# Optimization experiments

Hardware: AMD Instinct MI355X
Metric: run time of the kernel (lower is better)

The kernel has to match this reference:

```python
import jax, jax.numpy as jnp
import numpy as np

B, T, C, H, S = 4, 1024, 768, 12, 64  # batch, seq, emb_dim, n_heads, head_size
FF = 4 * C          # 3072, ff_hidden_size (required by SwiGLU input dim)
HID = int(8 * C / 3)  # 2048, SwiGLU hidden
EPS = 1e-6


def _rope_tables(seq_len, dim):
    # theta = 10000 ** (-2 * arange(0, dim, 2) / dim)  (note extra factor 2 vs standard RoPE)
    theta = 10000.0 ** (-2.0 * jnp.arange(0, dim, 2, dtype=jnp.float32) / dim)
    freqs = jnp.arange(seq_len, dtype=jnp.float32)[:, None] * theta  # [T, dim/2]
    cos = jnp.repeat(jnp.cos(freqs), 2, axis=-1)  # [T, dim]
    sin = jnp.repeat(jnp.sin(freqs), 2, axis=-1)
    return cos, sin


def _rope(x, cos, sin):
    # x: [..., T, S]; rotate pairs: even' = -odd, odd' = even
    rot = jnp.stack([-x[..., 1::2], x[..., 0::2]], axis=-1).reshape(x.shape)
    return x * cos + rot * sin


def _rmsnorm(x, gamma):
    # global scalar RMS over the whole tensor (faithful to torch.mean with no dim)
    return x / jnp.sqrt(EPS + jnp.mean(x * x)) * gamma


def _block(x, Wq, Wk, Wv, Wo, g1, g2, W1, b1, Ww, bw, Wg, bg, Wd, bd, W2, b2):
    Tlen = x.shape[1]
    cos, sin = _rope_tables(Tlen, S)
    # --- multi-head attention on rms1(x) ---
    h = _rmsnorm(x, g1)
    q = jnp.einsum('btc,hcs->bhts', h, Wq)
    k = jnp.einsum('btc,hcs->bhts', h, Wk)
    v = jnp.einsum('btc,hcs->bhts', h, Wv)
    rq = _rope(q, cos, sin)
    rk = _rope(k, cos, sin)
    scores = jnp.einsum('bhts,bhks->bhtk', rq, rk) * (C ** -0.5)  # scale by emb_dim, faithful
    causal = jnp.tril(jnp.ones((Tlen, Tlen), dtype=bool))
    scores = jnp.where(causal, scores, -jnp.inf)
    probs = jax.nn.softmax(scores, axis=-1)
    attn = jnp.einsum('bhtk,bhks->bhts', probs, v)
    attn = attn.transpose(0, 2, 1, 3).reshape(x.shape[0], Tlen, C)  # concat heads
    out = x + attn @ Wo
    # --- feed forward on rms2(out) ---
    h2 = _rmsnorm(out, g2)
    u = h2 @ W1 + b1                      # [B,T,FF]
    wx = u @ Ww + bw                      # [B,T,HID]
    vx = u @ Wg + bg
    ff = (wx * (vx * jax.nn.sigmoid(vx))) @ Wd + bd  # [B,T,FF]
    ff = ff @ W2 + b2                     # [B,T,C]
    return out + ff


def setup_inputs() -> dict:
    key = jax.random.key(0)
    ks = jax.random.split(key, 17)
    sd = 0.02
    return {
        'x':  jax.random.normal(ks[0], (B, T, C), jnp.float32),
        'Wq': jax.random.normal(ks[1], (H, C, S), jnp.float32) * sd,
        'Wk': jax.random.normal(ks[2], (H, C, S), jnp.float32) * sd,
        'Wv': jax.random.normal(ks[3], (H, C, S), jnp.float32) * sd,
        'Wo': jax.random.normal(ks[4], (C, C), jnp.float32) * sd,
        'g1': jnp.ones((C,), jnp.float32),
        'g2': jnp.ones((C,), jnp.float32),
        'W1': jax.random.normal(ks[5], (C, FF), jnp.float32) * sd,
        'b1': jnp.zeros((FF,), jnp.float32),
        'Ww': jax.random.normal(ks[6], (FF, HID), jnp.float32) * sd,
        'bw': jnp.zeros((HID,), jnp.float32),
        'Wg': jax.random.normal(ks[7], (FF, HID), jnp.float32) * sd,
        'bg': jnp.zeros((HID,), jnp.float32),
        'Wd': jax.random.normal(ks[8], (HID, FF), jnp.float32) * sd,
        'bd': jnp.zeros((FF,), jnp.float32),
        'W2': jax.random.normal(ks[9], (FF, C), jnp.float32) * sd,
        'b2': jnp.zeros((C,), jnp.float32),
    }


def reference(x, Wq, Wk, Wv, Wo, g1, g2, W1, b1, Ww, bw, Wg, bg, Wd, bd, W2, b2):
    return _block(x, Wq, Wk, Wv, Wo, g1, g2, W1, b1, Ww, bw, Wg, bg, Wd, bd, W2, b2)
```

## Files before the change

### kernel.cpp

```cpp
#include <hip/hip_runtime.h>
#include <math.h>

#define BB   4
#define TT   1024
#define CC   768
#define HH   12
#define SS   64
#define FFD  3072
#define HIDD 2048
#define NTOK (BB*TT)
#define EPSR 1e-6f

typedef __attribute__((ext_vector_type(8))) short bf16x8;
typedef __attribute__((ext_vector_type(4))) float f32x4;

__device__ __forceinline__ unsigned short f2bf(float f) {
    unsigned u = __float_as_uint(f);
    return (unsigned short)((u + 0x7FFFu + ((u >> 16) & 1u)) >> 16);
}
__device__ __forceinline__ float bfl(unsigned u) { return __uint_as_float(u << 16); }
__device__ __forceinline__ float bfh(unsigned u) { return __uint_as_float(u & 0xFFFF0000u); }
__device__ __forceinline__ unsigned pk2(float a, float b) {
    return (unsigned)f2bf(a) | ((unsigned)f2bf(b) << 16);
}

__device__ __forceinline__ void gload_lds16(const unsigned short* g, unsigned short* l) {
    __builtin_amdgcn_global_load_lds(
        (const __attribute__((address_space(1))) unsigned int*)g,
        (__attribute__((address_space(3))) unsigned int*)l, 16, 0, 0);
}

__global__ void k_scale_gamma_b(const float* __restrict__ x, const float* __restrict__ g,
                                const float* __restrict__ part, unsigned short* __restrict__ h,
                                int n8, float invn, int npart) {
    __shared__ float sm[256];
    float s = 0.f;
    for (int i = threadIdx.x; i < npart; i += 256) s += part[i];
    sm[threadIdx.x] = s;
    __syncthreads();
    for (int off = 128; off > 0; off >>= 1) {
        if (threadIdx.x < off) sm[threadIdx.x] += sm[threadIdx.x + off];
        __syncthreads();
    }
    float sc = 1.0f / sqrtf(EPSR + sm[0] * invn);
    int i = blockIdx.x * blockDim.x + threadIdx.x;
    if (i >= n8) return;
    float4 v0 = ((const float4*)x)[2*i];
    float4 v1 = ((const float4*)x)[2*i+1];
    int c = (i * 8) % CC;
    float4 g0 = *(const float4*)(g + c);
    float4 g1v = *(const float4*)(g + c + 4);
    uint4 r;
    r.x = pk2(v0.x*sc*g0.x,  v0.y*sc*g0.y);
    r.y = pk2(v0.z*sc*g0.z,  v0.w*sc*g0.w);
    r.z = pk2(v1.x*sc*g1v.x, v1.y*sc*g1v.y);
    r.w = pk2(v1.z*sc*g1v.z, v1.w*sc*g1v.w);
    ((uint4*)h)[i] = r;
}

#define TQKV 1728
#define TWO  576
#define TW1  2304
#define TWW  6144
#define TWD  6144
#define TW2  2304
#define J0 (TQKV)
#define J1 (J0 + TWO)
#define J2 (J1 + TW1)
#define J3 (J2 + TWW)
#define J4 (J3 + TWW)
#define J5 (J4 + TWD)
#define J6 (J5 + TW2)
#define J7 (J6 + 16)
#define J8 (J7 + 128)
#define JSUM 1024
#define J9 (J8 + JSUM)

__device__ __forceinline__ void wT_tile(float (*tl)[33], const float* __restrict__ W,
                                        unsigned short* __restrict__ Wt,
                                        int K, int N, int t, int tx, int ty) {
    int nk = K >> 5;
    int k0 = (t % nk) * 32, n0 = (t / nk) * 32;
#pragma unroll
    for (int i = 0; i < 4; ++i)
        tl[ty + i*8][tx] = W[(size_t)(k0 + ty + i*8) * N + n0 + tx];
    __syncthreads();
#pragma unroll
    for (int i = 0; i < 4; ++i)
        Wt[(size_t)(n0 + ty + i*8) * K + k0 + tx] = f2bf(tl[tx][ty + i*8]);
}

__device__ __forceinline__ void wT_tile_il(float (*tl)[33], const float* __restrict__ W,
                                           unsigned short* __restrict__ Wt,
                                           int K, int N, int t, int tx, int ty, int ofs) {
    int nk = K >> 5;
    int k0 = (t % nk) * 32, n0 = (t / nk) * 32;
#pragma unroll
    for (int i = 0; i < 4; ++i)
        tl[ty + i*8][tx] = W[(size_t)(k0 + ty + i*8) * N + n0 + tx];
    __syncthreads();
#pragma unroll
    for (int i = 0; i < 4; ++i) {
        int j = n0 + ty + i*8;
        int pr = ((j & ~15) << 1) + ofs*16 + (j & 15);
        Wt[(size_t)pr * K + k0 + tx] = f2bf(tl[tx][ty + i*8]);
    }
}

__global__ void k_prep(const float* __restrict__ Wq, const float* __restrict__ Wk,
                       const float* __restrict__ Wv, const float* __restrict__ Wo,
                       const float* __restrict__ W1, const float* __restrict__ Ww,
                       const float* __restrict__ Wg, const float* __restrict__ Wd,
                       const float* __restrict__ W2, const float* __restrict__ bw,
                       const float* __restrict__ bg, const float* __restrict__ x,
                       unsigned short* __restrict__ wqkvT, unsigned short* __restrict__ WoT,
                       unsigned short* __restrict__ W1T, unsigned short* __restrict__ WcatT,
                       unsigned short* __restrict__ WdT, unsigned short* __restrict__ W2T,
                       float* __restrict__ bcat, float* __restrict__ tab,
                       float* __restrict__ part) {
    __shared__ float tl[32][33];
    const int bid = blockIdx.x;
    const int tx = threadIdx.x & 31, ty = threadIdx.x >> 5;
    if (bid < J0) {
        int t = bid;
        int c0 = (t % 24) * 32;
        int s0 = ((t / 24) & 1) * 32;
        int z = t / 48, sel = z / HH, h = z % HH;
        const float* W = (sel == 0 ? Wq : (sel == 1 ? Wk : Wv)) + (size_t)h * CC * SS;
#pragma unroll
        for (int i = 0; i < 4; ++i)
            tl[ty + i*8][tx] = W[(size_t)(c0 + ty + i*8) * SS + s0 + tx];
        __syncthreads();
#pragma unroll
        for (int i = 0; i < 4; ++i)
            wqkvT[(size_t)(sel*CC + h*SS + s0 + ty + i*8) * CC + c0 + tx] = f2bf(tl[tx][ty + i*8]);
    } else if (bid < J1) {
        wT_tile(tl, Wo, WoT, CC, CC, bid - J0, tx, ty);
    } else if (bid < J2) {
        wT_tile(tl, W1, W1T, CC, FFD, bid - J1, tx, ty);
    } else if (bid < J3) {
        wT_tile_il(tl, Ww, WcatT, FFD, HIDD, bid - J2, tx, ty, 0);
    } else if (bid < J4) {
        wT_tile_il(tl, Wg, WcatT, FFD, HIDD, bid - J3, tx, ty, 1);
    } else if (bid < J5) {
        wT_tile(tl, Wd, WdT, HIDD, FFD, bid - J4, tx, ty);
    } else if (bid < J6) {
        wT_tile(tl, W2, W2T, FFD, CC, bid - J5, tx, ty);
    } else if (bid < J7) {
        int ip = (bid - J6) * 256 + threadIdx.x;
        int lg = ((ip >> 5) << 4) + (ip & 15);
        bcat[ip] = ((ip >> 4) & 1) ? bg[lg] : bw[lg];
    } else if (bid < J8) {
        int i = (bid - J7) * 256 + threadIdx.x;
        int t = i >> 5, j = i & 31;
        float th = expf(-(float)j * 0.5756462732485115f);
        float ang = (float)t * th;
        tab[2*i]   = cosf(ang);
        tab[2*i+1] = sinf(ang);
    } else {
        float* sm = &tl[0][0];
        const int pb = bid - J8;
        const int n4 = NTOK * CC / 4;
        float s = 0.f;
        int stride = JSUM * 256;
        for (int i = pb * 256 + threadIdx.x; i < n4; i += stride) {
            float4 v = ((const float4*)x)[i];
            s += v.x*v.x + v.y*v.y + v.z*v.z + v.w*v.w;
        }
        sm[threadIdx.x] = s;
        __syncthreads();
        for (int off = 128; off > 0; off >>= 1) {
            if (threadIdx.x < off) sm[threadIdx.x] += sm[threadIdx.x + off];
            __syncthreads();
        }
        if (threadIdx.x == 0) part[pb] = sm[0];
    }
}

__global__ void k_rope_vt(unsigned short* __restrict__ qkv, const float* __restrict__ tab,
                          unsigned short* __restrict__ vtg) {
    const int bid = blockIdx.x;
    if (bid < 6144) {
        int i = bid * 256 + threadIdx.x;
        int j  = i & 31;
        int h  = (i >> 5) % HH;
        int bt = i / (32 * HH);
        int t  = bt & (TT - 1);
        float cs = tab[(t*32 + j)*2];
        float sn = tab[(t*32 + j)*2 + 1];
        size_t base = (size_t)bt * (3*CC) + h * SS + 2*j;
        unsigned q = *(unsigned*)(qkv + base);
        float qe = bfl(q), qo = bfh(q);
        *(unsigned*)(qkv + base) = pk2(qe*cs - qo*sn, qo*cs + qe*sn);
        unsigned k = *(unsigned*)(qkv + base + CC);
        float ke = bfl(k), ko = bfh(k);
        *(unsigned*)(qkv + base + CC) = pk2(ke*cs - ko*sn, ko*cs + ke*sn);
    } else {
        int b2 = bid - 6144;
        int bh = b2 >> 3, ty = b2 & 7;
        int b = bh / HH, h = bh % HH;
        int d = threadIdx.x & 63, tq = threadIdx.x >> 6;
        int t0 = ty * 128 + tq * 32;
        const unsigned short* src = qkv + (size_t)(b*TT + t0)*(3*CC) + 2*CC + h*SS + d;
        unsigned v[16];
#pragma unroll
        for (int e = 0; e < 16; ++e) {
            unsigned lo = src[(size_t)(2*e)*(3*CC)];
            unsigned hi = src[(size_t)(2*e+1)*(3*CC)];
            v[e] = (lo & 0xFFFFu) | (hi << 16);
        }
        uint4* dst = (uint4*)(vtg + ((size_t)bh*64 + d)*TT + t0);
#pragma unroll
        for (int q = 0; q < 4; ++q)
            dst[q] = make_uint4(v[q*4], v[q*4+1], v[q*4+2], v[q*4+3]);
    }
}

template<bool BIAS, bool RES, bool OUTB, bool SSQ>
__global__ __launch_bounds__(256) void k_gemm_bf16(
    const unsigned short* __restrict__ A, const unsigned short* __restrict__ Bt,
    const float* __restrict__ bias, const float* __restrict__ res,
    void* __restrict__ Cv, int M, int N, int K, float* __restrict__ ssq_part)
{
    __shared__ unsigned short As[2][128*32];
    __shared__ unsigned short Bs[2][128*32];
    __shared__ float smr[256];
    const int tid  = threadIdx.x;
    const int w    = tid >> 6, lane = tid & 63;
    const int wr   = w >> 1,  wc   = w & 1;
    const int row0 = blockIdx.y * 128, col0 = blockIdx.x * 128;

    f32x4 acc[4][4];
#pragma unroll
    for (int m = 0; m < 4; ++m)
#pragma unroll
        for (int n = 0; n < 4; ++n) acc[m][n] = (f32x4){0.f, 0.f, 0.f, 0.f};

    const int lr4 = lane >> 2;
    const int scb = lane & 3;

    auto stage = [&](int t, int buf) {
#pragma unroll
        for (int i = 0; i < 2; ++i) {
            int lr = w * 32 + i * 16 + lr4;
            int cbs = scb ^ ((lr >> 1) & 3);
            const unsigned short* ga = A + (size_t)(row0 + lr) * K + t * 32 + cbs * 8;
            gload_lds16(ga, &As[buf][(w * 32 + i * 16) * 32]);
            const unsigned short* gb = Bt + (size_t)(col0 + lr) * K + t * 32 + cbs * 8;
            gload_lds16(gb, &Bs[buf][(w * 32 + i * 16) * 32]);
        }
    };

    const int nt = K / 32;
    stage(0, 0);
    int cur = 0;
    const int fr = lane & 15, fq = lane >> 4;
    for (int t = 0; t < nt; ++t) {
        __syncthreads();
        if (t + 1 < nt) stage(t + 1, cur ^ 1);
        bf16x8 af[4], bf[4];
#pragma unroll
        for (int m = 0; m < 4; ++m) {
            int ra = wr * 64 + m * 16 + fr;
            af[m] = *(const bf16x8*)&As[cur][ra * 32 + (fq ^ ((ra >> 1) & 3)) * 8];
            int rb = wc * 64 + m * 16 + fr;
            bf[m] = *(const bf16x8*)&Bs[cur][rb * 32 + (fq ^ ((rb >> 1) & 3)) * 8];
        }
#pragma unroll
        for (int m = 0; m < 4; ++m)
#pragma unroll
            for (int n = 0; n < 4; ++n)
                acc[m][n] = __builtin_amdgcn_mfma_f32_16x16x32_bf16(af[m], bf[n], acc[m][n], 0, 0, 0);
        cur ^= 1;
    }

    float ssq = 0.f;
#pragma unroll
    for (int m = 0; m < 4; ++m) {
#pragma unroll
        for (int n = 0; n < 4; ++n) {
            int col = col0 + wc * 64 + n * 16 + fr;
            float bv = BIAS ? bias[col] : 0.f;
#pragma unroll
            for (int j = 0; j < 4; ++j) {
                int row = row0 + wr * 64 + m * 16 + fq * 4 + j;
                size_t off = (size_t)row * N + col;
                float v = acc[m][n][j] + bv;
                if (RES) v += res[off];
                if (OUTB) ((unsigned short*)Cv)[off] = f2bf(v);
                else      ((float*)Cv)[off] = v;
                if (SSQ) ssq += v * v;
            }
        }
    }
    if (SSQ) {
        smr[tid] = ssq;
        __syncthreads();
        for (int off = 128; off > 0; off >>= 1) {
            if (tid < off) smr[tid] += smr[tid + off];
            __syncthreads();
        }
        if (tid == 0) ssq_part[blockIdx.y * gridDim.x + blockIdx.x] = smr[0];
    }
}

#define GSTEP(s_, DOSTAGE, GATE)                                                  \
    {                                                                             \
        const int st_ = (s_) & 3;                                                 \
        const unsigned short* pa_ = &ringA[st_][0];                               \
        const unsigned short* pb_ = &ringB[st_][0];                               \
        bf16x8 af[8], bv[4];                                                      \
        _Pragma("unroll")                                                         \
        for (int m = 0; m < 8; ++m)                                               \
            af[m] = *(const bf16x8*)&pa_[offA[m]];                                \
        _Pragma("unroll")                                                         \
        for (int n = 0; n < 4; ++n)                                               \
            bv[n] = *(const bf16x8*)&pb_[offB[n]];                                \
        if (DOSTAGE) { stageA((s_) + 3); stageB((s_) + 3); }                      \
        asm volatile("s_waitcnt lgkmcnt(0)" ::: "memory");                        \
        __builtin_amdgcn_sched_barrier(0);                                        \
        __builtin_amdgcn_s_setprio(1);                                            \
        _Pragma("unroll")                                                         \
        for (int m = 0; m < 8; ++m)                                               \
            _Pragma("unroll")                                                     \
            for (int n = 0; n < 4; ++n)                                           \
                acc[m][n] = __builtin_amdgcn_mfma_f32_16x16x32_bf16(              \
                    af[m], bv[n], acc[m][n], 0, 0, 0);                            \
        __builtin_amdgcn_s_setprio(0);                                            \
        asm volatile("s_waitcnt " GATE ::: "memory");                             \
        __builtin_amdgcn_sched_barrier(0);                                        \
        __builtin_amdgcn_s_barrier();                                             \
    }

template<bool BIAS, bool SWIGLU>
__global__ __launch_bounds__(512, 2) void k_gemm256(
    const unsigned short* __restrict__ A, const unsigned short* __restrict__ Bt,
    const float* __restrict__ bias, unsigned short* __restrict__ C,
    int M, int N, int K)
{
    __shared__ __align__(16) unsigned short ringA[4][256*32];
    __shared__ __align__(16) unsigned short ringB[4][256*32];
    const int tid = threadIdx.x;
    const int w = tid >> 6, lane = tid & 63;
    const int wm = w >> 2, wn = w & 3;
    const int fr = lane & 15, fq = lane >> 4;

    const int nwg = gridDim.x * gridDim.y;
    const int bid = blockIdx.y * gridDim.x + blockIdx.x;
    const int cpx = nwg >> 3;
    const int sbid = (bid & 7) * cpx + (bid >> 3);
    const int row0 = (sbid / gridDim.x) * 256;
    const int col0 = (sbid % gridDim.x) * 256;

    f32x4 acc[8][4];
#pragma unroll
    for (int m = 0; m < 8; ++m)
#pragma unroll
        for (int n = 0; n < 4; ++n) acc[m][n] = (f32x4){0.f, 0.f, 0.f, 0.f};

    const int c0 = tid, c1 = 512 + tid;
    const int r0 = c0 >> 2, p0 = ((c0 & 3) ^ ((r0 >> 1) & 3)) * 8;
    const int r1 = c1 >> 2, p1 = ((c1 & 3) ^ ((r1 >> 1) & 3)) * 8;
    const unsigned short* aS0 = A  + (size_t)(row0 + r0) * K + p0;
    const unsigned short* aS1 = A  + (size_t)(row0 + r1) * K + p1;
    const unsigned short* bS0 = Bt + (size_t)(col0 + r0) * K + p0;
    const unsigned short* bS1 = Bt + (size_t)(col0 + r1) * K + p1;
    const int dL = w * 512;
    auto stageA = [&](int t) {
        const int st = t & 3;
        const int kb = t * 32;
        gload_lds16(aS0 + kb, &ringA[st][dL]);
        gload_lds16(aS1 + kb, &ringA[st][4096 + dL]);
    };
    auto stageB = [&](int t) {
        const int st = t & 3;
        const int kb = t * 32;
        gload_lds16(bS0 + kb, &ringB[st][dL]);
        gload_lds16(bS1 + kb, &ringB[st][4096 + dL]);
    };

    int offA[8], offB[4];
#pragma unroll
    for (int m = 0; m < 8; ++m) {
        int ra = wm*128 + m*16 + fr;
        offA[m] = ra*32 + (fq ^ ((ra >> 1) & 3))*8;
    }
#pragma unroll
    for (int n = 0; n < 4; ++n) {
        int rb = wn*64 + n*16 + fr;
        offB[n] = rb*32 + (fq ^ ((rb >> 1) & 3))*8;
    }

    const int S = K >> 5;
    stageA(0); stageB(0); stageA(1); stageB(1); stageA(2); stageB(2);
    asm volatile("s_waitcnt vmcnt(8)" ::: "memory");
    __builtin_amdgcn_s_barrier();
    int s = 0;
    for (; s < S - 3; ++s) GSTEP(s, true, "vmcnt(8)");
    GSTEP(s, false, "vmcnt(4)"); ++s;
    GSTEP(s, false, "vmcnt(0)"); ++s;
    GSTEP(s, false, "vmcnt(0)");

    if (SWIGLU) {
#pragma unroll
        for (int m = 0; m < 8; ++m) {
#pragma unroll
            for (int n = 0; n < 4; n += 2) {
                int colw = col0 + wn*64 + n*16 + fr;
                float bw_ = BIAS ? bias[colw] : 0.f;
                float bg_ = BIAS ? bias[colw + 16] : 0.f;
                int colo = ((colw >> 5) << 4) + (colw & 15);
#pragma unroll
                for (int j = 0; j < 4; ++j) {
                    int row = row0 + wm*128 + m*16 + fq*4 + j;
                    float wx = acc[m][n][j] + bw_;
                    float vx = acc[m][n+1][j] + bg_;
                    float sw = wx * vx / (1.f + __expf(-vx));
                    C[(size_t)row * (N >> 1) + colo] = f2bf(sw);
                }
            }
        }
    } else {
#pragma unroll
        for (int m = 0; m < 8; ++m) {
#pragma unroll
            for (int n = 0; n < 4; ++n) {
                int col = col0 + wn*64 + n*16 + fr;
                float bvb = BIAS ? bias[col] : 0.f;
#pragma unroll
                for (int j = 0; j < 4; ++j) {
                    int row = row0 + wm*128 + m*16 + fq*4 + j;
                    C[(size_t)row * N + col] = f2bf(acc[m][n][j] + bvb);
                }
            }
        }
    }
}

__global__ __launch_bounds__(256) void k_attn_mfma(
    const unsigned short* __restrict__ qkv, const unsigned short* __restrict__ vtg,
    unsigned short* __restrict__ attn)
{
    __shared__ __align__(16) unsigned short Ks[2][64*64];
    __shared__ __align__(16) unsigned short Vs[2][64*64];
    __shared__ __align__(16) unsigned short Ps[4][16*72];
    const int tid = threadIdx.x;
    const int w = tid >> 6, lane = tid & 63;
    const int fr = lane & 15, fq = lane >> 4;
    const int bh = blockIdx.x, b = bh / HH, h = bh % HH;
    const int qb = blockIdx.y * 64;
    const int nkt = qb / 64 + 1;
    const float scale = 0.03608439182435161f;

    bf16x8 qf[2];
    {
        const unsigned short* qp = qkv + (size_t)(b*TT + qb + w*16 + fr)*(3*CC) + h*SS + fq*8;
        qf[0] = *(const bf16x8*)qp;
        qf[1] = *(const bf16x8*)(qp + 32);
    }

    auto stage = [&](int kt, int buf) {
        const unsigned short* kbase = qkv + (size_t)(b*TT + kt*64)*(3*CC) + CC + h*SS;
        const unsigned short* vbase = vtg + ((size_t)bh*64)*TT + kt*64;
#pragma unroll
        for (int p = 0; p < 2; ++p) {
            int s = p*256 + tid;
            int row = s >> 3;
            int blk = (s & 7) ^ (row & 7);
            gload_lds16(kbase + (size_t)row*(3*CC) + blk*8, &Ks[buf][(p*256 + w*64)*8]);
            gload_lds16(vbase + (size_t)row*TT + blk*8,     &Vs[buf][(p*256 + w*64)*8]);
        }
    };

    float m[4] = {-INFINITY, -INFINITY, -INFINITY, -INFINITY};
    float l[4] = {0.f, 0.f, 0.f, 0.f};
    f32x4 oacc[4];
#pragma unroll
    for (int n = 0; n < 4; ++n) oacc[n] = (f32x4){0.f, 0.f, 0.f, 0.f};

    stage(0, 0);
    int cur = 0;
    for (int kt = 0; kt < nkt; ++kt) {
        __syncthreads();
        if (kt + 1 < nkt) stage(kt + 1, cur ^ 1);

        f32x4 sacc[4];
#pragma unroll
        for (int n = 0; n < 4; ++n) sacc[n] = (f32x4){0.f, 0.f, 0.f, 0.f};
#pragma unroll
        for (int ks = 0; ks < 2; ++ks) {
#pragma unroll
            for (int n = 0; n < 4; ++n) {
                int row = n*16 + fr;
                bf16x8 kf = *(const bf16x8*)&Ks[cur][row*64 + ((ks*4 + fq) ^ (row & 7))*8];
                sacc[n] = __builtin_amdgcn_mfma_f32_16x16x32_bf16(qf[ks], kf, sacc[n], 0, 0, 0);
            }
        }

        float sv[4][4];
        const bool lastt = (kt == nkt - 1);
        const int qloc = w*16 + fq*4;
#pragma unroll
        for (int n = 0; n < 4; ++n) {
            int kloc = n*16 + fr;
#pragma unroll
            for (int j = 0; j < 4; ++j) {
                float vv = sacc[n][j] * scale;
                if (lastt && kloc > qloc + j) vv = -INFINITY;
                sv[j][n] = vv;
            }
        }
        float mx[4], ls[4];
#pragma unroll
        for (int j = 0; j < 4; ++j)
            mx[j] = fmaxf(fmaxf(sv[j][0], sv[j][1]), fmaxf(sv[j][2], sv[j][3]));
#pragma unroll
        for (int d = 1; d < 16; d <<= 1)
#pragma unroll
            for (int j = 0; j < 4; ++j) mx[j] = fmaxf(mx[j], __shfl_xor(mx[j], d));
        float corr[4];
#pragma unroll
        for (int j = 0; j < 4; ++j) {
            float nm = fmaxf(m[j], mx[j]);
            corr[j] = __expf(m[j] - nm);
            m[j] = nm;
        }
#pragma unroll
        for (int j = 0; j < 4; ++j) {
            float s0 = 0.f;
#pragma unroll
            for (int n = 0; n < 4; ++n) {
                float p = __expf(sv[j][n] - m[j]);
                sv[j][n] = p;
                s0 += p;
            }
            ls[j] = s0;
        }
#pragma unroll
        for (int d = 1; d < 16; d <<= 1)
#pragma unroll
            for (int j = 0; j < 4; ++j) ls[j] += __shfl_xor(ls[j], d);
#pragma unroll
        for (int j = 0; j < 4; ++j) l[j] = l[j]*corr[j] + ls[j];
#pragma unroll
        for (int n = 0; n < 4; ++n)
#pragma unroll
            for (int j = 0; j < 4; ++j) oacc[n][j] *= corr[j];

#pragma unroll
        for (int j = 0; j < 4; ++j)
#pragma unroll
            for (int n = 0; n < 4; ++n)
                Ps[w][(fq*4 + j)*72 + n*16 + fr] = f2bf(sv[j][n]);

#pragma unroll
        for (int ks = 0; ks < 2; ++ks) {
            bf16x8 pf = *(const bf16x8*)&Ps[w][fr*72 + ks*32 + fq*8];
#pragma unroll
            for (int n = 0; n < 4; ++n) {
                int row = n*16 + fr;
                bf16x8 vf = *(const bf16x8*)&Vs[cur][row*64 + ((ks*4 + fq) ^ (row & 7))*8];
                oacc[n] = __builtin_amdgcn_mfma_f32_16x16x32_bf16(pf, vf, oacc[n], 0, 0, 0);
            }
        }
        cur ^= 1;
    }

    float inv[4];
#pragma unroll
    for (int j = 0; j < 4; ++j) inv[j] = 1.0f / l[j];
#pragma unroll
    for (int n = 0; n < 4; ++n)
#pragma unroll
        for (int j = 0; j < 4; ++j) {
            size_t off = (size_t)(b*TT + qb + w*16 + fq*4 + j)*CC + h*SS + n*16 + fr;
            attn[off] = f2bf(oacc[n][j] * inv[j]);
        }
}

extern "C" void kernel_launch(void* const* d_in, const int* in_sizes, int n_in,
                              void* d_out, int out_size, void* d_ws, size_t ws_size,
                              hipStream_t stream)
{
    const float* x  = (const float*)d_in[0];
    const float* Wq = (const float*)d_in[1];
    const float* Wk = (const float*)d_in[2];
    const float* Wv = (const float*)d_in[3];
    const float* Wo = (const float*)d_in[4];
    const float* g1 = (const float*)d_in[5];
    const float* g2 = (const float*)d_in[6];
    const float* W1 = (const float*)d_in[7];
    const float* b1 = (const float*)d_in[8];
    const float* Ww = (const float*)d_in[9];
    const float* bw = (const float*)d_in[10];
    const float* Wg = (const float*)d_in[11];
    const float* bg = (const float*)d_in[12];
    const float* Wd = (const float*)d_in[13];
    const float* bd = (const float*)d_in[14];
    const float* W2 = (const float*)d_in[15];
    const float* b2 = (const float*)d_in[16];
    float* out = (float*)d_out;

    char* p = (char*)d_ws;
    auto alloc = [&](size_t bytes) { char* r = p; p += (bytes + 255) & ~(size_t)255; return r; };

    float*          part   = (float*)alloc(4096);
    float*          tab    = (float*)alloc((size_t)TT*32*2*4);
    float*          bcat   = (float*)alloc((size_t)2*HIDD*4);
    unsigned short* hb     = (unsigned short*)alloc((size_t)NTOK*CC*2);
    unsigned short* wqkvT  = (unsigned short*)alloc((size_t)3*CC*CC*2);
    unsigned short* qkvb   = (unsigned short*)alloc((size_t)NTOK*3*CC*2);
    unsigned short* vtg    = (unsigned short*)alloc((size_t)BB*HH*SS*TT*2);
    unsigned short* attnb  = (unsigned short*)alloc((size_t)NTOK*CC*2);
    unsigned short* WoT    = (unsigned short*)alloc((size_t)CC*CC*2);
    unsigned short* W1T    = (unsigned short*)alloc((size_t)FFD*CC*2);
    unsigned short* ub     = (unsigned short*)alloc((size_t)NTOK*FFD*2);
    unsigned short* WcatT  = (unsigned short*)alloc((size_t)2*HIDD*FFD*2);
    unsigned short* swb    = (unsigned short*)alloc((size_t)NTOK*HIDD*2);
    unsigned short* WdT    = (unsigned short*)alloc((size_t)FFD*HIDD*2);
    unsigned short* W2T    = (unsigned short*)alloc((size_t)CC*FFD*2);

    const int n = NTOK * CC;

    k_prep<<<J9, 256, 0, stream>>>(Wq, Wk, Wv, Wo, W1, Ww, Wg, Wd, W2, bw, bg, x,
                                   wqkvT, WoT, W1T, WcatT, WdT, W2T, bcat, tab, part);

    k_scale_gamma_b<<<(n/8)/256, 256, 0, stream>>>(x, g1, part, hb, n/8,
                                                   1.0f/(float)n, JSUM);

    k_gemm256<false,false><<<dim3(3*CC/256, NTOK/256), 512, 0, stream>>>(
        hb, wqkvT, nullptr, qkvb, NTOK, 3*CC, CC);
    k_rope_vt<<<6144 + 384, 256, 0, stream>>>(qkvb, tab, vtg);

    k_attn_mfma<<<dim3(BB*HH, TT/64), 256, 0, stream>>>(qkvb, vtg, attnb);

    k_gemm_bf16<false,true,false,true><<<dim3(CC/128, NTOK/128), 256, 0, stream>>>(
        attnb, WoT, nullptr, x, out, NTOK, CC, CC, part);

    k_scale_gamma_b<<<(n/8)/256, 256, 0, stream>>>(out, g2, part, hb, n/8,
                                                   1.0f/(float)n, (CC/128)*(NTOK/128));

    k_gemm256<true,false><<<dim3(FFD/256, NTOK/256), 512, 0, stream>>>(
        hb, W1T, b1, ub, NTOK, FFD, CC);
    k_gemm256<true,true><<<dim3(2*HIDD/256, NTOK/256), 512, 0, stream>>>(
        ub, WcatT, bcat, swb, NTOK, 2*HIDD, FFD);
    k_gemm256<true,false><<<dim3(FFD/256, NTOK/256), 512, 0, stream>>>(
        swb, WdT, bd, ub, NTOK, FFD, HIDD);
    k_gemm_bf16<true,true,false,false><<<dim3(CC/128, NTOK/128), 256, 0, stream>>>(
        ub, W2T, b2, out, out, NTOK, CC, FFD, nullptr);
}
```

Baseline: 377.6 us.

## Shrink gemm256 tile to 128x256 with 3-stage ring for higher occupancy

Halves the M tile of the large bf16 GEMM kernel from 256 to 128 rows, cuts the LDS ring from 4 to 3 stages, and raises the launch-bounds occupancy hint from 2 to 4 blocks. The grids double in the M direction, which gives more workgroups on the many CUs and lower register and LDS use per block. In exchange, each block reuses its loaded B tile over fewer rows, adding global traffic, and the pipeline is shallower, leaving less latency hiding per block.

```diff
diff --git a/kernel.cpp b/kernel.cpp
--- a/kernel.cpp
+++ b/kernel.cpp
@@ -304,24 +304,23 @@
     }
 }
 
-#define GSTEP(s_, DOSTAGE, GATE)                                                  \
+#define GSTEP(SL, STG, SNUM, DOSTAGE, GATE)                                       \
     {                                                                             \
-        const int st_ = (s_) & 3;                                                 \
-        const unsigned short* pa_ = &ringA[st_][0];                               \
-        const unsigned short* pb_ = &ringB[st_][0];                               \
-        bf16x8 af[8], bv[4];                                                      \
+        const unsigned short* pa_ = &ringA[SL][0];                                \
+        const unsigned short* pb_ = &ringB[SL][0];                                \
+        bf16x8 af[4], bv[4];                                                      \
         _Pragma("unroll")                                                         \
-        for (int m = 0; m < 8; ++m)                                               \
+        for (int m = 0; m < 4; ++m)                                               \
             af[m] = *(const bf16x8*)&pa_[offA[m]];                                \
         _Pragma("unroll")                                                         \
         for (int n = 0; n < 4; ++n)                                               \
             bv[n] = *(const bf16x8*)&pb_[offB[n]];                                \
-        if (DOSTAGE) { stageA((s_) + 3); stageB((s_) + 3); }                      \
+        if (DOSTAGE) { stageA(SNUM, STG); stageB(SNUM, STG); }                    \
         asm volatile("s_waitcnt lgkmcnt(0)" ::: "memory");                        \
         __builtin_amdgcn_sched_barrier(0);                                        \
         __builtin_amdgcn_s_setprio(1);                                            \
         _Pragma("unroll")                                                         \
-        for (int m = 0; m < 8; ++m)                                               \
+        for (int m = 0; m < 4; ++m)                                               \
             _Pragma("unroll")                                                     \
             for (int n = 0; n < 4; ++n)                                           \
                 acc[m][n] = __builtin_amdgcn_mfma_f32_16x16x32_bf16(              \
@@ -333,13 +332,13 @@
     }
 
 template<bool BIAS, bool SWIGLU>
-__global__ __launch_bounds__(512, 2) void k_gemm256(
+__global__ __launch_bounds__(512, 4) void k_gemm256(
     const unsigned short* __restrict__ A, const unsigned short* __restrict__ Bt,
     const float* __restrict__ bias, unsigned short* __restrict__ C,
     int M, int N, int K)
 {
-    __shared__ __align__(16) unsigned short ringA[4][256*32];
-    __shared__ __align__(16) unsigned short ringB[4][256*32];
+    __shared__ __align__(16) unsigned short ringA[3][128*32];
+    __shared__ __align__(16) unsigned short ringB[3][256*32];
     const int tid = threadIdx.x;
     const int w = tid >> 6, lane = tid & 63;
     const int wm = w >> 2, wn = w & 3;
@@ -349,12 +348,12 @@
     const int bid = blockIdx.y * gridDim.x + blockIdx.x;
     const int cpx = nwg >> 3;
     const int sbid = (bid & 7) * cpx + (bid >> 3);
-    const int row0 = (sbid / gridDim.x) * 256;
+    const int row0 = (sbid / gridDim.x) * 128;
     const int col0 = (sbid % gridDim.x) * 256;
 
-    f32x4 acc[8][4];
-#pragma unroll
-    for (int m = 0; m < 8; ++m)
+    f32x4 acc[4][4];
+#pragma unroll
+    for (int m = 0; m < 4; ++m)
 #pragma unroll
         for (int n = 0; n < 4; ++n) acc[m][n] = (f32x4){0.f, 0.f, 0.f, 0.f};
 
@@ -362,27 +361,22 @@
     const int r0 = c0 >> 2, p0 = ((c0 & 3) ^ ((r0 >> 1) & 3)) * 8;
     const int r1 = c1 >> 2, p1 = ((c1 & 3) ^ ((r1 >> 1) & 3)) * 8;
     const unsigned short* aS0 = A  + (size_t)(row0 + r0) * K + p0;
-    const unsigned short* aS1 = A  + (size_t)(row0 + r1) * K + p1;
     const unsigned short* bS0 = Bt + (size_t)(col0 + r0) * K + p0;
     const unsigned short* bS1 = Bt + (size_t)(col0 + r1) * K + p1;
     const int dL = w * 512;
-    auto stageA = [&](int t) {
-        const int st = t & 3;
+    auto stageA = [&](int t, int sl) {
+        gload_lds16(aS0 + t * 32, &ringA[sl][dL]);
+    };
+    auto stageB = [&](int t, int sl) {
         const int kb = t * 32;
-        gload_lds16(aS0 + kb, &ringA[st][dL]);
-        gload_lds16(aS1 + kb, &ringA[st][4096 + dL]);
+        gload_lds16(bS0 + kb, &ringB[sl][dL]);
+        gload_lds16(bS1 + kb, &ringB[sl][4096 + dL]);
     };
-    auto stageB = [&](int t) {
-        const int st = t & 3;
-        const int kb = t * 32;
-        gload_lds16(bS0 + kb, &ringB[st][dL]);
-        gload_lds16(bS1 + kb, &ringB[st][4096 + dL]);
-    };
-
-    int offA[8], offB[4];
-#pragma unroll
-    for (int m = 0; m < 8; ++m) {
-        int ra = wm*128 + m*16 + fr;
+
+    int offA[4], offB[4];
+#pragma unroll
+    for (int m = 0; m < 4; ++m) {
+        int ra = wm*64 + m*16 + fr;
         offA[m] = ra*32 + (fq ^ ((ra >> 1) & 3))*8;
     }
 #pragma unroll
@@ -392,18 +386,23 @@
     }
 
     const int S = K >> 5;
-    stageA(0); stageB(0); stageA(1); stageB(1); stageA(2); stageB(2);
-    asm volatile("s_waitcnt vmcnt(8)" ::: "memory");
+    stageA(0, 0); stageB(0, 0); stageA(1, 1); stageB(1, 1);
+    asm volatile("s_waitcnt vmcnt(3)" ::: "memory");
     __builtin_amdgcn_s_barrier();
-    int s = 0;
-    for (; s < S - 3; ++s) GSTEP(s, true, "vmcnt(8)");
-    GSTEP(s, false, "vmcnt(4)"); ++s;
-    GSTEP(s, false, "vmcnt(0)"); ++s;
-    GSTEP(s, false, "vmcnt(0)");
+
+    int sl = 0, stg = 2;
+    for (int s = 0; s < S - 2; ++s) {
+        GSTEP(sl, stg, s + 2, true, "vmcnt(3)");
+        sl  = (sl  == 2) ? 0 : sl  + 1;
+        stg = (stg == 2) ? 0 : stg + 1;
+    }
+    GSTEP(sl, 0, 0, false, "vmcnt(0)");
+    sl = (sl == 2) ? 0 : sl + 1;
+    GSTEP(sl, 0, 0, false, "vmcnt(0)");
 
     if (SWIGLU) {
 #pragma unroll
-        for (int m = 0; m < 8; ++m) {
+        for (int m = 0; m < 4; ++m) {
 #pragma unroll
             for (int n = 0; n < 4; n += 2) {
                 int colw = col0 + wn*64 + n*16 + fr;
@@ -412,7 +411,7 @@
                 int colo = ((colw >> 5) << 4) + (colw & 15);
 #pragma unroll
                 for (int j = 0; j < 4; ++j) {
-                    int row = row0 + wm*128 + m*16 + fq*4 + j;
+                    int row = row0 + wm*64 + m*16 + fq*4 + j;
                     float wx = acc[m][n][j] + bw_;
                     float vx = acc[m][n+1][j] + bg_;
                     float sw = wx * vx / (1.f + __expf(-vx));
@@ -422,14 +421,14 @@
         }
     } else {
 #pragma unroll
-        for (int m = 0; m < 8; ++m) {
+        for (int m = 0; m < 4; ++m) {
 #pragma unroll
             for (int n = 0; n < 4; ++n) {
                 int col = col0 + wn*64 + n*16 + fr;
                 float bvb = BIAS ? bias[col] : 0.f;
 #pragma unroll
                 for (int j = 0; j < 4; ++j) {
-                    int row = row0 + wm*128 + m*16 + fq*4 + j;
+                    int row = row0 + wm*64 + m*16 + fq*4 + j;
                     C[(size_t)row * N + col] = f2bf(acc[m][n][j] + bvb);
                 }
             }
@@ -628,7 +627,7 @@
     k_scale_gamma_b<<<(n/8)/256, 256, 0, stream>>>(x, g1, part, hb, n/8,
                                                    1.0f/(float)n, JSUM);
 
-    k_gemm256<false,false><<<dim3(3*CC/256, NTOK/256), 512, 0, stream>>>(
+    k_gemm256<false,false><<<dim3(3*CC/256, NTOK/128), 512, 0, stream>>>(
         hb, wqkvT, nullptr, qkvb, NTOK, 3*CC, CC);
     k_rope_vt<<<6144 + 384, 256, 0, stream>>>(qkvb, tab, vtg);
 
@@ -640,11 +639,11 @@
     k_scale_gamma_b<<<(n/8)/256, 256, 0, stream>>>(out, g2, part, hb, n/8,
                                                    1.0f/(float)n, (CC/128)*(NTOK/128));
 
-    k_gemm256<true,false><<<dim3(FFD/256, NTOK/256), 512, 0, stream>>>(
+    k_gemm256<true,false><<<dim3(FFD/256, NTOK/128), 512, 0, stream>>>(
         hb, W1T, b1, ub, NTOK, FFD, CC);
-    k_gemm256<true,true><<<dim3(2*HIDD/256, NTOK/256), 512, 0, stream>>>(
+    k_gemm256<true,true><<<dim3(2*HIDD/256, NTOK/128), 512, 0, stream>>>(
         ub, WcatT, bcat, swb, NTOK, 2*HIDD, FFD);
-    k_gemm256<true,false><<<dim3(FFD/256, NTOK/256), 512, 0, stream>>>(
+    k_gemm256<true,false><<<dim3(FFD/256, NTOK/128), 512, 0, stream>>>(
         swb, WdT, bd, ub, NTOK, FFD, HIDD);
     k_gemm_bf16<true,true,false,false><<<dim3(CC/128, NTOK/128), 256, 0, stream>>>(
         ub, W2T, b2, out, out, NTOK, CC, FFD, nullptr);
```

Result: slower. 402.7 us (+6.6%).
